# Kernel tuning notes

Hardware: AMD Instinct MI355X
Metric: run time of the kernel (lower is better)

## Reference

```python
import jax, jax.numpy as jnp
import numpy as np

SEQ, D_IN, D_OUT, RANK, N_ADAPTERS = 8192, 4096, 4096, 16, 8


def setup_inputs() -> dict:
    key = jax.random.key(0)
    ks = jax.random.split(key, 7)
    return {
        "x": jax.random.normal(ks[0], (SEQ, D_IN), jnp.float32),
        "weight": jax.random.normal(ks[1], (D_IN, D_OUT), jnp.float32) * (D_IN ** -0.5),
        "bias": jax.random.normal(ks[2], (D_OUT,), jnp.float32),
        "A_buffer": jax.random.normal(ks[3], (N_ADAPTERS, RANK, D_IN), jnp.float32) * (D_IN ** -0.5),
        "B_buffer": jax.random.normal(ks[4], (N_ADAPTERS, D_OUT, RANK), jnp.float32) * (RANK ** -0.5),
        "scalings": jax.random.uniform(ks[5], (SEQ,), jnp.float32, 0.5, 2.0),
        "token_indices": jax.random.randint(ks[6], (SEQ,), 0, N_ADAPTERS, jnp.int32),
    }


def reference(x, weight, bias, A_buffer, B_buffer, scalings, token_indices):
    # Base linear layer: [S, D_in] @ [D_in, D_out] + bias
    base_output = x @ weight + bias
    n_adapters = A_buffer.shape[0]
    delta = jnp.zeros_like(base_output)
    # Grouped LoRA GEMM: per-adapter small GEMMs, masked scatter back per token.
    for e in range(n_adapters):
        # run_lora_a_gemm: x @ A[e]^T with per-token scaling -> [S, rank]
        a_out = (x @ A_buffer[e].T) * scalings[:, None]
        # run_lora_b_gemm: a_out @ B[e]^T -> [S, D_out]
        b_out = a_out @ B_buffer[e].T
        delta = delta + jnp.where((token_indices == e)[:, None], b_out, 0.0)
    return base_output + delta
```

## Files before the change

kernel.cpp:

```cpp
#include <hip/hip_runtime.h>
#include <hip/hip_bf16.h>
#include <cstdint>

#define SEQ   8192
#define DIN   4096
#define DOUT  4096
#define RANK  16
#define NAD   8
#define KC    (DIN + NAD*RANK)

using f32x4  = __attribute__((ext_vector_type(4))) float;
using bf16x8 = __attribute__((ext_vector_type(8))) short;

__device__ __forceinline__ unsigned short f2bf(float f) {
  union { float f; uint32_t u; } v; v.f = f;
  return (unsigned short)((v.u + 0x7fffu + ((v.u >> 16) & 1u)) >> 16);
}

__device__ __forceinline__ void async_copy16(void* lds, const void* gmem) {
  __builtin_amdgcn_global_load_lds(
      (__attribute__((address_space(1))) void*)(uintptr_t)gmem,
      (__attribute__((address_space(3))) void*)(uint32_t)(uintptr_t)lds,
      16, 0, 0);
}


__global__ void cvt_x_kernel(const float* __restrict__ x, unsigned short* __restrict__ xcat) {
  const int64_t nchunks = (int64_t)SEQ * DIN / 8;
  for (int64_t c = (int64_t)blockIdx.x * blockDim.x + threadIdx.x; c < nchunks;
       c += (int64_t)gridDim.x * blockDim.x) {
    int64_t base = c * 8;
    int s = (int)(base >> 12);
    int k = (int)(base & (DIN - 1));
    float4 p = *(const float4*)(x + base);
    float4 q = *(const float4*)(x + base + 4);
    union { unsigned short h[8]; int4 v; } o;
    o.h[0]=f2bf(p.x); o.h[1]=f2bf(p.y); o.h[2]=f2bf(p.z); o.h[3]=f2bf(p.w);
    o.h[4]=f2bf(q.x); o.h[5]=f2bf(q.y); o.h[6]=f2bf(q.z); o.h[7]=f2bf(q.w);
    *(int4*)(xcat + (int64_t)s * KC + k) = o.v;
  }
}

__global__ void cvt_a_kernel(const float* __restrict__ a, unsigned short* __restrict__ abf) {
  int c = blockIdx.x * 256 + threadIdx.x;
  int64_t base = (int64_t)c * 8;
  float4 p = *(const float4*)(a + base);
  float4 q = *(const float4*)(a + base + 4);
  union { unsigned short h[8]; int4 v; } o;
  o.h[0]=f2bf(p.x); o.h[1]=f2bf(p.y); o.h[2]=f2bf(p.z); o.h[3]=f2bf(p.w);
  o.h[4]=f2bf(q.x); o.h[5]=f2bf(q.y); o.h[6]=f2bf(q.z); o.h[7]=f2bf(q.w);
  *(int4*)(abf + base) = o.v;
}

__global__ void cvt_w_kernel(const float* __restrict__ w, unsigned short* __restrict__ wcat) {
  int t  = threadIdx.x;
  int bn = blockIdx.x & 127;
  int bk = blockIdx.x >> 7;
  int n = bn * 32 + (t & 31);
  int k = bk * 64 + (t >> 5) * 8;
  union { unsigned short h[8]; int4 v; } o;
#pragma unroll
  for (int j = 0; j < 8; j++)
    o.h[j] = f2bf(w[(int64_t)(k + j) * DOUT + n]);
  *(int4*)(wcat + (int64_t)n * KC + k) = o.v;
}

__global__ void cvt_b_kernel(const float* __restrict__ Bbuf, unsigned short* __restrict__ wcat) {
  int idx = blockIdx.x * 256 + threadIdx.x;
  int n = idx >> 7, er = idx & 127;
  int e = er >> 4, r = er & 15;
  float v = Bbuf[((int64_t)e * DOUT + n) * RANK + r];
  wcat[(int64_t)n * KC + DIN + er] = f2bf(v);
}

__global__ __launch_bounds__(256) void gemm_lora_a(
    const unsigned short* __restrict__ A,
    const unsigned short* __restrict__ Bb,
    float* __restrict__ aout) {
  constexpr int BK = 64;
  __shared__ unsigned short sA[64 * BK];
  __shared__ unsigned short sB[128 * BK];
  int tid = threadIdx.x, wave = tid >> 6, lane = tid & 63;
  int quad = lane >> 4, l16 = lane & 15;
  int mb = blockIdx.x & 127;
  int sp = blockIdx.x >> 7;
  int row0 = mb * 64;
  int kbase = sp * (DIN / 2);
  int wm = wave >> 1, wn = wave & 1;
  int f8 = l16 & 7;

  const f32x4 zero = {0.f, 0.f, 0.f, 0.f};
  f32x4 acc[2][4];
#pragma unroll
  for (int i = 0; i < 2; i++)
#pragma unroll
    for (int j = 0; j < 4; j++) acc[i][j] = zero;

  for (int kt = 0; kt < (DIN / 2) / BK; ++kt) {
    int k0 = kbase + kt * BK;
#pragma unroll
    for (int i = 0; i < 2; i++) {
      int c = i * 256 + tid;
      int r = c >> 3, kc = ((c & 7) ^ (r & 7)) * 8;
      async_copy16(&sA[c * 8], A + (int64_t)(row0 + r) * KC + k0 + kc);
    }
#pragma unroll
    for (int i = 0; i < 4; i++) {
      int c = i * 256 + tid;
      int r = c >> 3, kc = ((c & 7) ^ (r & 7)) * 8;
      async_copy16(&sB[c * 8], Bb + (int64_t)r * DIN + k0 + kc);
    }
    __syncthreads();
#pragma unroll
    for (int ks = 0; ks < 2; ks++) {
      bf16x8 af[2], bfr[4];
      int qq = ks * 4 + quad;
      int qp = (qq ^ f8) * 8;
#pragma unroll
      for (int mi = 0; mi < 2; mi++)
        af[mi] = *(const bf16x8*)&sA[(wm * 32 + mi * 16 + l16) * BK + qp];
#pragma unroll
      for (int ni = 0; ni < 4; ni++)
        bfr[ni] = *(const bf16x8*)&sB[(wn * 64 + ni * 16 + l16) * BK + qp];
#pragma unroll
      for (int mi = 0; mi < 2; mi++)
#pragma unroll
        for (int ni = 0; ni < 4; ni++)
          acc[mi][ni] = __builtin_amdgcn_mfma_f32_16x16x32_bf16(af[mi], bfr[ni], acc[mi][ni], 0, 0, 0);
    }
    __syncthreads();
  }

  float* op = aout + (int64_t)sp * SEQ * 128;
#pragma unroll
  for (int ni = 0; ni < 4; ni++) {
    int er = wn * 64 + ni * 16 + l16;
#pragma unroll
    for (int mi = 0; mi < 2; mi++) {
      int s0 = row0 + wm * 32 + mi * 16 + quad * 4;
#pragma unroll
      for (int r = 0; r < 4; r++)
        op[(int64_t)(s0 + r) * 128 + er] = acc[mi][ni][r];
    }
  }
}

__global__ void lora_combine(const float* __restrict__ aout, const float* __restrict__ scal,
                             const int* __restrict__ tok, unsigned short* __restrict__ xcat) {
  int idx = blockIdx.x * 256 + threadIdx.x;
  int s = idx >> 7, er = idx & 127;
  float v = aout[idx] + aout[idx + (int64_t)SEQ * 128];
  v *= scal[s];
  v = ((er >> 4) == tok[s]) ? v : 0.0f;
  xcat[(int64_t)s * KC + DIN + er] = f2bf(v);
}

__global__ __launch_bounds__(256) void gemm_main(
    const unsigned short* __restrict__ A,
    const unsigned short* __restrict__ B,
    const float* __restrict__ bias,
    float* __restrict__ out) {
  constexpr int BK = 32;
  constexpr int KITERS = KC / BK;
  __shared__ unsigned short sA[128 * BK];
  __shared__ unsigned short sB[128 * BK];
  int tid = threadIdx.x, wave = tid >> 6, lane = tid & 63;
  int quad = lane >> 4, l16 = lane & 15;
  int bn = blockIdx.x & 31, bm = blockIdx.x >> 5;
  int row0 = bm * 128, col0 = bn * 128;
  int wm = wave >> 1, wn = wave & 1;
  int fR = (l16 + (l16 >> 2)) & 3;
  int qp = (quad ^ fR) * 8;

  const f32x4 zero = {0.f, 0.f, 0.f, 0.f};
  f32x4 acc[4][4];
#pragma unroll
  for (int i = 0; i < 4; i++)
#pragma unroll
    for (int j = 0; j < 4; j++) acc[i][j] = zero;

  const unsigned short* Ab = A + (int64_t)row0 * KC;
  const unsigned short* Bb = B + (int64_t)col0 * KC;

  for (int kt = 0; kt < KITERS; ++kt) {
    int k0 = kt * BK;
#pragma unroll
    for (int i = 0; i < 2; i++) {
      int c = i * 256 + tid;
      int r = c >> 2;
      int kc = ((c & 3) ^ ((r + (r >> 2)) & 3)) * 8;
      async_copy16(&sA[c * 8], Ab + (int64_t)r * KC + k0 + kc);
      async_copy16(&sB[c * 8], Bb + (int64_t)r * KC + k0 + kc);
    }
    __syncthreads();
    bf16x8 af[4], bfr[4];
#pragma unroll
    for (int mi = 0; mi < 4; mi++)
      af[mi] = *(const bf16x8*)&sA[(wm * 64 + mi * 16 + l16) * BK + qp];
#pragma unroll
    for (int ni = 0; ni < 4; ni++)
      bfr[ni] = *(const bf16x8*)&sB[(wn * 64 + ni * 16 + l16) * BK + qp];
#pragma unroll
    for (int mi = 0; mi < 4; mi++)
#pragma unroll
      for (int ni = 0; ni < 4; ni++)
        acc[mi][ni] = __builtin_amdgcn_mfma_f32_16x16x32_bf16(af[mi], bfr[ni], acc[mi][ni], 0, 0, 0);
    __syncthreads();
  }

#pragma unroll
  for (int ni = 0; ni < 4; ni++) {
    int col = col0 + wn * 64 + ni * 16 + l16;
    float bv = bias[col];
#pragma unroll
    for (int mi = 0; mi < 4; mi++) {
      int rbase = row0 + wm * 64 + mi * 16 + quad * 4;
#pragma unroll
      for (int r = 0; r < 4; r++)
        out[(int64_t)(rbase + r) * DOUT + col] = acc[mi][ni][r] + bv;
    }
  }
}

__global__ void fb_aout(const float* __restrict__ x, const float* __restrict__ Abuf,
                        const float* __restrict__ scal, const int* __restrict__ tok,
                        float* __restrict__ aout) {
  int s = blockIdx.x;
  int e = tok[s];
  __shared__ float red[256];
  for (int r = 0; r < RANK; ++r) {
    float p = 0.f;
    for (int k = threadIdx.x; k < DIN; k += 256)
      p += x[(int64_t)s * DIN + k] * Abuf[((int64_t)e * RANK + r) * DIN + k];
    red[threadIdx.x] = p;
    __syncthreads();
    for (int off = 128; off > 0; off >>= 1) {
      if (threadIdx.x < off) red[threadIdx.x] += red[threadIdx.x + off];
      __syncthreads();
    }
    if (threadIdx.x == 0) aout[s * RANK + r] = red[0] * scal[s];
    __syncthreads();
  }
}
__global__ void fb_out(const float* __restrict__ x, const float* __restrict__ w,
                       const float* __restrict__ bias, const float* __restrict__ Bbuf,
                       const int* __restrict__ tok, const float* __restrict__ aout,
                       float* __restrict__ out) {
  int64_t idx = (int64_t)blockIdx.x * blockDim.x + threadIdx.x;
  int s = (int)(idx >> 12), n = (int)(idx & (DOUT - 1));
  float accv = bias[n];
  for (int k = 0; k < DIN; ++k)
    accv += x[(int64_t)s * DIN + k] * w[(int64_t)k * DOUT + n];
  int e = tok[s];
  float d = 0.f;
  for (int r = 0; r < RANK; ++r)
    d += aout[s * RANK + r] * Bbuf[((int64_t)e * DOUT + n) * RANK + r];
  out[idx] = accv + d;
}

extern "C" void kernel_launch(void* const* d_in, const int* in_sizes, int n_in,
                              void* d_out, int out_size, void* d_ws, size_t ws_size,
                              hipStream_t stream) {
  const float* x    = (const float*)d_in[0];
  const float* w    = (const float*)d_in[1];
  const float* bias = (const float*)d_in[2];
  const float* Abuf = (const float*)d_in[3];
  const float* Bbuf = (const float*)d_in[4];
  const float* scal = (const float*)d_in[5];
  const int*   tok  = (const int*)d_in[6];
  float* out = (float*)d_out;

  const size_t xcat_b = (size_t)SEQ * KC * 2;
  const size_t wcat_b = (size_t)DOUT * KC * 2;
  const size_t abf_b  = (size_t)NAD * RANK * DIN * 2;
  const size_t aout_b = (size_t)2 * SEQ * 128 * 4;

  if (ws_size >= xcat_b + wcat_b + abf_b + aout_b) {
    unsigned short* xcat = (unsigned short*)d_ws;
    unsigned short* wcat = (unsigned short*)((char*)d_ws + xcat_b);
    unsigned short* abf  = (unsigned short*)((char*)d_ws + xcat_b + wcat_b);
    float*          aout = (float*)((char*)d_ws + xcat_b + wcat_b + abf_b);
    cvt_x_kernel<<<4096, 256, 0, stream>>>(x, xcat);
    cvt_w_kernel<<<8192, 256, 0, stream>>>(w, wcat);
    cvt_b_kernel<<<(DOUT * 128) / 256, 256, 0, stream>>>(Bbuf, wcat);
    cvt_a_kernel<<<(NAD * RANK * DIN / 8) / 256, 256, 0, stream>>>(Abuf, abf);
    gemm_lora_a<<<256, 256, 0, stream>>>(xcat, abf, aout);
    lora_combine<<<(SEQ * 128) / 256, 256, 0, stream>>>(aout, scal, tok, xcat);
    gemm_main<<<(SEQ / 128) * (DOUT / 128), 256, 0, stream>>>(xcat, wcat, bias, out);
  } else {
    float* aout = (float*)d_ws;
    fb_aout<<<SEQ, 256, 0, stream>>>(x, Abuf, scal, tok, aout);
    fb_out<<<(int)(((int64_t)SEQ * DOUT) / 256), 256, 0, stream>>>(x, w, bias, Bbuf, tok, aout, out);
  }
}
```

Baseline: 636.2 us.

## Double-buffer LDS tiles and switch main GEMM to 32x32x16 MFMA

The main bf16 GEMM now keeps two LDS buffers. It issues the async global-to-LDS copy for the next K tile before computing on the current one, which removes one barrier per iteration and overlaps loads with MFMA work. The inner product moves from 16x16x32 to 32x32x16 bf16 MFMA with 2x2 accumulator tiles of 16 floats each, which cuts LDS fragment reads per MFMA flop. The trade-off is twice the LDS, different register pressure, and reliance on the single remaining barrier for correctness of the async copies.

```diff
diff --git a/kernel.cpp b/kernel.cpp
--- a/kernel.cpp
+++ b/kernel.cpp
@@ -9,8 +9,9 @@
 #define NAD   8
 #define KC    (DIN + NAD*RANK)
 
-using f32x4  = __attribute__((ext_vector_type(4))) float;
-using bf16x8 = __attribute__((ext_vector_type(8))) short;
+using f32x4   = __attribute__((ext_vector_type(4))) float;
+using f32x16  = __attribute__((ext_vector_type(16))) float;
+using bf16x8  = __attribute__((ext_vector_type(8))) short;
 
 __device__ __forceinline__ unsigned short f2bf(float f) {
   union { float f; uint32_t u; } v; v.f = f;
@@ -162,62 +163,76 @@
     float* __restrict__ out) {
   constexpr int BK = 32;
   constexpr int KITERS = KC / BK;
-  __shared__ unsigned short sA[128 * BK];
-  __shared__ unsigned short sB[128 * BK];
+  __shared__ unsigned short sA[2][128 * BK];
+  __shared__ unsigned short sB[2][128 * BK];
   int tid = threadIdx.x, wave = tid >> 6, lane = tid & 63;
-  int quad = lane >> 4, l16 = lane & 15;
+  int l32 = lane & 31, lh = lane >> 5;
   int bn = blockIdx.x & 31, bm = blockIdx.x >> 5;
   int row0 = bm * 128, col0 = bn * 128;
   int wm = wave >> 1, wn = wave & 1;
-  int fR = (l16 + (l16 >> 2)) & 3;
-  int qp = (quad ^ fR) * 8;
-
-  const f32x4 zero = {0.f, 0.f, 0.f, 0.f};
-  f32x4 acc[4][4];
-#pragma unroll
-  for (int i = 0; i < 4; i++)
-#pragma unroll
-    for (int j = 0; j < 4; j++) acc[i][j] = zero;
+  int fR = (l32 + (l32 >> 2)) & 3;
+
+  f32x16 acc[2][2];
+#pragma unroll
+  for (int i = 0; i < 2; i++)
+#pragma unroll
+    for (int j = 0; j < 2; j++)
+#pragma unroll
+      for (int r = 0; r < 16; r++) acc[i][j][r] = 0.f;
 
   const unsigned short* Ab = A + (int64_t)row0 * KC;
   const unsigned short* Bb = B + (int64_t)col0 * KC;
 
+  int c0 = tid,        r0 = c0 >> 2, kc0 = ((c0 & 3) ^ ((r0 + (r0 >> 2)) & 3)) * 8;
+  int c1 = 256 + tid,  r1 = c1 >> 2, kc1 = ((c1 & 3) ^ ((r1 + (r1 >> 2)) & 3)) * 8;
+
+#define STAGE(buf, k0)                                                        \
+  do {                                                                        \
+    async_copy16(&sA[buf][c0 * 8], Ab + (int64_t)r0 * KC + (k0) + kc0);       \
+    async_copy16(&sB[buf][c0 * 8], Bb + (int64_t)r0 * KC + (k0) + kc0);       \
+    async_copy16(&sA[buf][c1 * 8], Ab + (int64_t)r1 * KC + (k0) + kc1);       \
+    async_copy16(&sB[buf][c1 * 8], Bb + (int64_t)r1 * KC + (k0) + kc1);       \
+  } while (0)
+
+  STAGE(0, 0);
+  int cur = 0;
   for (int kt = 0; kt < KITERS; ++kt) {
-    int k0 = kt * BK;
-#pragma unroll
-    for (int i = 0; i < 2; i++) {
-      int c = i * 256 + tid;
-      int r = c >> 2;
-      int kc = ((c & 3) ^ ((r + (r >> 2)) & 3)) * 8;
-      async_copy16(&sA[c * 8], Ab + (int64_t)r * KC + k0 + kc);
-      async_copy16(&sB[c * 8], Bb + (int64_t)r * KC + k0 + kc);
-    }
-    __syncthreads();
-    bf16x8 af[4], bfr[4];
-#pragma unroll
-    for (int mi = 0; mi < 4; mi++)
-      af[mi] = *(const bf16x8*)&sA[(wm * 64 + mi * 16 + l16) * BK + qp];
-#pragma unroll
-    for (int ni = 0; ni < 4; ni++)
-      bfr[ni] = *(const bf16x8*)&sB[(wn * 64 + ni * 16 + l16) * BK + qp];
-#pragma unroll
-    for (int mi = 0; mi < 4; mi++)
-#pragma unroll
-      for (int ni = 0; ni < 4; ni++)
-        acc[mi][ni] = __builtin_amdgcn_mfma_f32_16x16x32_bf16(af[mi], bfr[ni], acc[mi][ni], 0, 0, 0);
-    __syncthreads();
-  }
-
-#pragma unroll
-  for (int ni = 0; ni < 4; ni++) {
-    int col = col0 + wn * 64 + ni * 16 + l16;
+    __syncthreads();
+    if (kt + 1 < KITERS) STAGE(cur ^ 1, (kt + 1) * BK);
+    bf16x8 af[2][2], bfr[2][2];
+#pragma unroll
+    for (int s = 0; s < 2; s++) {
+      int qp = ((2 * s + lh) ^ fR) * 8;
+#pragma unroll
+      for (int mi = 0; mi < 2; mi++)
+        af[mi][s] = *(const bf16x8*)&sA[cur][(wm * 64 + mi * 32 + l32) * BK + qp];
+#pragma unroll
+      for (int ni = 0; ni < 2; ni++)
+        bfr[ni][s] = *(const bf16x8*)&sB[cur][(wn * 64 + ni * 32 + l32) * BK + qp];
+    }
+#pragma unroll
+    for (int s = 0; s < 2; s++)
+#pragma unroll
+      for (int mi = 0; mi < 2; mi++)
+#pragma unroll
+        for (int ni = 0; ni < 2; ni++)
+          acc[mi][ni] = __builtin_amdgcn_mfma_f32_32x32x16_bf16(af[mi][s], bfr[ni][s], acc[mi][ni], 0, 0, 0);
+    cur ^= 1;
+  }
+#undef STAGE
+
+#pragma unroll
+  for (int ni = 0; ni < 2; ni++) {
+    int col = col0 + wn * 64 + ni * 32 + l32;
     float bv = bias[col];
 #pragma unroll
-    for (int mi = 0; mi < 4; mi++) {
-      int rbase = row0 + wm * 64 + mi * 16 + quad * 4;
-#pragma unroll
-      for (int r = 0; r < 4; r++)
-        out[(int64_t)(rbase + r) * DOUT + col] = acc[mi][ni][r] + bv;
+    for (int mi = 0; mi < 2; mi++) {
+      int rbase = row0 + wm * 64 + mi * 32 + 4 * lh;
+#pragma unroll
+      for (int g = 0; g < 4; g++)
+#pragma unroll
+        for (int r4 = 0; r4 < 4; r4++)
+          out[(int64_t)(rbase + 8 * g + r4) * DOUT + col] = acc[mi][ni][g * 4 + r4] + bv;
     }
   }
 }
```

Result: no change. 647.7 us (+1.8%).
